# Performance work log

Measured on AMD Instinct MI355X. Metric: run time of the kernel, lower is better.

## Reference

```python
import jax, jax.numpy as jnp
import numpy as np

LEAKY_SLOPE = 0.01  # torch nn.LeakyReLU default


def leaky_relu(x):
    return jnp.where(x >= 0, x, LEAKY_SLOPE * x)


def rgcn_conv(x, edge_index, edge_type, w_rel, w_root, b_conv):
    # PyG RGCNConv: out = x @ W_root + b + sum_r mean_{edges of rel r into i}(x_src @ W_r)
    n = x.shape[0]
    src, dst = edge_index[0], edge_index[1]
    out = x @ w_root + b_conv
    num_rel = w_rel.shape[0]
    for r in range(num_rel):  # small fixed relation count
        mask = (edge_type == r)
        msg = x[src] @ w_rel[r]                      # [E, H]
        msg = jnp.where(mask[:, None], msg, 0.0)
        agg = jax.ops.segment_sum(msg, dst, num_segments=n)          # [N, H]
        cnt = jax.ops.segment_sum(mask.astype(x.dtype), dst, num_segments=n)
        out = out + agg / jnp.maximum(cnt, 1.0)[:, None]             # mean aggr
    return out


def setup_inputs() -> dict:
    key = jax.random.key(0)
    ks = jax.random.split(key, 10)
    N, E, D_IN, H, OUT, R = 50000, 600000, 768, 128, 3, 2
    s_in = 1.0 / np.sqrt(D_IN)
    s_h = 1.0 / np.sqrt(H)
    return {
        "feature": jax.random.normal(ks[0], (N, D_IN), dtype=jnp.float32),
        "edge_index": jax.random.randint(ks[1], (2, E), 0, N, dtype=jnp.int64),
        "edge_type": jax.random.randint(ks[2], (E,), 0, R, dtype=jnp.int64),
        "w_in": jax.random.uniform(ks[3], (D_IN, H), jnp.float32, -s_in, s_in),
        "b_in": jax.random.uniform(ks[4], (H,), jnp.float32, -s_in, s_in),
        "w_rel": jax.random.uniform(ks[5], (R, H, H), jnp.float32, -s_h, s_h),
        "w_root": jax.random.uniform(ks[6], (H, H), jnp.float32, -s_h, s_h),
        "b_conv": jnp.zeros((H,), jnp.float32),
        "w_out": jax.random.uniform(ks[7], (H, OUT), jnp.float32, -s_h, s_h),
        "b_out": jax.random.uniform(ks[8], (OUT,), jnp.float32, -s_h, s_h),
    }


def reference(feature, edge_index, edge_type, w_in, b_in, w_rel, w_root, b_conv, w_out, b_out):
    x = leaky_relu(feature @ w_in + b_in)
    # NOTE: original forward applies rgcn1 twice (shared weights); dropout is
    # identity at inference; rgcn2/linear_relu_output1 are unused.
    x = rgcn_conv(x, edge_index, edge_type, w_rel, w_root, b_conv)
    x = rgcn_conv(x, edge_index, edge_type, w_rel, w_root, b_conv)
    return x @ w_out + b_out
```

## Files before the change

### kernel.cpp

```cpp
#include <hip/hip_runtime.h>

#define H 128
#define CAP 64

typedef _Float16 f16x8 __attribute__((ext_vector_type(8)));
typedef _Float16 f16x2 __attribute__((ext_vector_type(2)));
typedef float    f32x4 __attribute__((ext_vector_type(4)));

__global__ __launch_bounds__(256) void prep_all(const float* __restrict__ w_in,
    const float* __restrict__ w_root, const float* __restrict__ w_rel,
    const float* __restrict__ b_conv, const float* __restrict__ w_out,
    const float* __restrict__ b_out, _Float16* __restrict__ wInT,
    _Float16* __restrict__ wcatT, float* __restrict__ wfin,
    float* __restrict__ bfin, int K, int OUT)
{
    int idx = blockIdx.x * 256 + threadIdx.x;
    int tot1 = K * H;
    if (idx < tot1) {
        int k = idx >> 7, c = idx & 127;
        int o = ((k >> 3) << 10) + (c << 3) + (k & 7);
        wInT[o] = (_Float16)w_in[idx];
        return;
    }
    int i2 = idx - tot1;
    if (i2 < H * 384) {
        int c = i2 / 384, k = i2 - c * 384;
        float v;
        if (k < 128)      v = w_root[(size_t)k * H + c];
        else if (k < 256) v = w_rel[(size_t)(k - 128) * H + c];
        else              v = w_rel[(size_t)H * H + (size_t)(k - 256) * H + c];
        wcatT[i2] = (_Float16)v;
        return;
    }
    int i3 = i2 - H * 384;
    int nw = 3 * H * OUT;
    if (i3 < nw) {
        int mk = i3 / OUT, c = i3 - mk * OUT;
        int m = mk >> 7, k = mk & 127;
        const float* W = (m == 0) ? w_root : (w_rel + (size_t)(m - 1) * H * H);
        float s = 0.f;
        for (int j = 0; j < H; j++)
            s += W[(size_t)k * H + j] * w_out[(size_t)j * OUT + c];
        wfin[(size_t)mk * OUT + c] = s;
    } else if (i3 < nw + OUT) {
        int c = i3 - nw;
        float s = b_out[c];
        for (int j = 0; j < H; j++) s += b_conv[j] * w_out[(size_t)j * OUT + c];
        bfin[c] = s;
    }
}

__device__ __forceinline__ f16x8 cvt8(float4 v0, float4 v1) {
    f16x8 t;
    t[0] = (_Float16)v0.x; t[1] = (_Float16)v0.y; t[2] = (_Float16)v0.z; t[3] = (_Float16)v0.w;
    t[4] = (_Float16)v1.x; t[5] = (_Float16)v1.y; t[6] = (_Float16)v1.z; t[7] = (_Float16)v1.w;
    return t;
}

__global__ __launch_bounds__(256, 2) void gemm_hist(const float* __restrict__ A,
    const _Float16* __restrict__ WP, const float* __restrict__ bias,
    _Float16* __restrict__ C16, int M, int K, int ldc, int gemmBlocks,
    const int* __restrict__ esrc, const int* __restrict__ edst,
    const int* __restrict__ et, int* __restrict__ cnt, int* __restrict__ elist,
    int E, int N)
{
    __shared__ float As[2][4][2048];

    if ((int)blockIdx.x >= gemmBlocks) {
        int e = (blockIdx.x - gemmBlocks) * 256 + threadIdx.x;
        if (e < E) {
            int s = esrc[e], d = edst[e], t = et[e];
            int b = t * N + d;
            int pos = atomicAdd(&cnt[b], 1);
            if (pos < CAP)
                __builtin_nontemporal_store(s, &elist[(size_t)b * CAP + pos]);
        }
        return;
    }

    const int tid = threadIdx.x;
    const int w   = tid >> 6;
    const int l   = tid & 63;
    const int l15 = l & 15;
    const int q   = l >> 4;
    const int brow = blockIdx.x * 64;
    const int wr   = w * 16;

    const int lh  = l >> 5;
    const int l31 = l & 31;

    const _Float16* bp = WP + ((size_t)q * H + l15) * 8;

    float bj[8];
#pragma unroll
    for (int j = 0; j < 8; j++) bj[j] = bias[j * 16 + l15];

    f32x4 acc[8];
    const f32x4 z4 = {0.f, 0.f, 0.f, 0.f};
#pragma unroll
    for (int j = 0; j < 8; j++) acc[j] = z4;

    const int chunks = K / 128;

#define STAGE(c, nbuf)                                                          \
    {                                                                           \
        _Pragma("unroll")                                                       \
        for (int i = 0; i < 8; i++) {                                           \
            int r  = 2 * i + lh;                                                \
            int gr = brow + wr + r; if (gr >= M) gr = M - 1;                    \
            int cg = l31 ^ (r & 7);                                             \
            const float* ga = A + (size_t)gr * K + (c) * 128 + cg * 4;          \
            __builtin_amdgcn_global_load_lds(                                   \
                (const __attribute__((address_space(1))) void*)ga,              \
                (__attribute__((address_space(3))) void*)&As[nbuf][w][i * 256], \
                16, 0, 0);                                                      \
        }                                                                       \
    }

    STAGE(0, 0);
    __syncthreads();

    for (int c = 0; c < chunks; c++) {
        if (c + 1 < chunks) STAGE(c + 1, (c + 1) & 1);

        const float* wbuf = As[c & 1][w];
#pragma unroll
        for (int ks = 0; ks < 4; ks++) {
            const int sl = ks * 4 + q;
            const int xr = l15 & 7;
            const int p0 = (2 * sl) ^ xr;
            const int p1 = (2 * sl + 1) ^ xr;
            float4 lo = *(const float4*)&wbuf[l15 * 128 + p0 * 4];
            float4 hi = *(const float4*)&wbuf[l15 * 128 + p1 * 4];
            f16x8 af = cvt8(lo, hi);
            const _Float16* bks = bp + (size_t)(c * 4 + ks) * 4096;
            f16x8 bf[8];
#pragma unroll
            for (int j = 0; j < 8; j++) bf[j] = *(const f16x8*)(bks + j * 128);
#pragma unroll
            for (int j = 0; j < 8; j++)
                acc[j] = __builtin_amdgcn_mfma_f32_16x16x32_f16(af, bf[j], acc[j], 0, 0, 0);
        }
        __syncthreads();
    }
#undef STAGE

#pragma unroll
    for (int rg = 0; rg < 4; rg++) {
        int row = brow + wr + q * 4 + rg;
        if (row < M) {
#pragma unroll
            for (int j = 0; j < 8; j++) {
                float v = acc[j][rg] + bj[j];
                v = (v >= 0.f) ? v : 0.01f * v;
                C16[(size_t)row * ldc + j * 16 + l15] = (_Float16)v;
            }
        }
    }
}

__global__ __launch_bounds__(256) void fused_l1(const _Float16* __restrict__ X1,
    const _Float16* __restrict__ WT, const float* __restrict__ bias,
    const int* __restrict__ elist, const int* __restrict__ cnt,
    _Float16* __restrict__ X2, int N)
{
    __shared__ _Float16 Ml[16][264];

    const int w   = threadIdx.x >> 6;
    const int l   = threadIdx.x & 63;
    const int l15 = l & 15;
    const int q   = l >> 4;
    const int r0  = blockIdx.x * 16;

    const int eo   = l >> 4;
    const int e2   = eo & 1;
    const int half = l >> 5;
    const int c8   = l15 * 8;

    const f16x8 zv = {};
#pragma unroll
    for (int i = 0; i < 4; i++) {
        const int rl = w * 4 + i;
        const int r  = r0 + rl;
        float acc[8];
#pragma unroll
        for (int j = 0; j < 8; j++) acc[j] = 0.f;
        float inv = 0.f;
        if (r < N) {
            int dr = cnt[(size_t)half * N + r];
            int d  = dr < CAP ? dr : CAP;
            inv = dr > 0 ? 1.f / (float)dr : 0.f;
            const int* lst = elist + ((size_t)half * N + r) * CAP;
            for (int p = e2; p < d; p += 8) {
                int p1 = p + 2, p2 = p + 4, p3 = p + 6;
                int s0 = lst[p];
                f16x8 v0 = *(const f16x8*)&X1[(size_t)s0 * H + c8];
                f16x8 v1 = zv, v2 = zv, v3 = zv;
                if (p1 < d) { int s = lst[p1]; v1 = *(const f16x8*)&X1[(size_t)s * H + c8]; }
                if (p2 < d) { int s = lst[p2]; v2 = *(const f16x8*)&X1[(size_t)s * H + c8]; }
                if (p3 < d) { int s = lst[p3]; v3 = *(const f16x8*)&X1[(size_t)s * H + c8]; }
#pragma unroll
                for (int j = 0; j < 8; j++)
                    acc[j] += (float)v0[j] + (float)v1[j] + (float)v2[j] + (float)v3[j];
            }
        }
#pragma unroll
        for (int j = 0; j < 8; j++) {
            acc[j] += __shfl_xor(acc[j], 16);
            acc[j] *= inv;
        }
        if (r < N && (eo == 0 || eo == 2)) {
            f16x8 o;
#pragma unroll
            for (int j = 0; j < 8; j++) o[j] = (_Float16)acc[j];
            *(f16x8*)&Ml[rl][half * 128 + c8] = o;
        }
    }
    __syncthreads();

    int gr = r0 + l15; if (gr >= N) gr = N - 1;
    f16x8 xf[12];
    {
        const _Float16* xp = X1 + (size_t)gr * H + q * 8;
#pragma unroll
        for (int c = 0; c < 4; c++) xf[c] = *(const f16x8*)(xp + c * 32);
#pragma unroll
        for (int c = 4; c < 12; c++) xf[c] = *(const f16x8*)&Ml[l15][(c - 4) * 32 + q * 8];
    }

    const f32x4 z4 = {0.f, 0.f, 0.f, 0.f};
#pragma unroll
    for (int cf = 0; cf < 2; cf++) {
        const int col = w * 32 + cf * 16 + l15;
        f16x8 bf[12];
        const _Float16* wpp = WT + (size_t)col * 384 + q * 8;
#pragma unroll
        for (int c = 0; c < 12; c++) bf[c] = *(const f16x8*)(wpp + c * 32);
        f32x4 a0 = z4;
#pragma unroll
        for (int c = 0; c < 12; c++)
            a0 = __builtin_amdgcn_mfma_f32_16x16x32_f16(xf[c], bf[c], a0, 0, 0, 0);
        const float bj = bias[col];
#pragma unroll
        for (int rg = 0; rg < 4; rg++) {
            int row = r0 + q * 4 + rg;
            if (row < N) X2[(size_t)row * H + col] = (_Float16)(a0[rg] + bj);
        }
    }
}

__global__ __launch_bounds__(256) void proj9(const _Float16* __restrict__ X2,
    const float* __restrict__ wfin, float* __restrict__ P, int N)
{
    int row = blockIdx.x * 4 + (threadIdx.x >> 6);
    int l   = threadIdx.x & 63;
    if (row >= N) return;

    f16x2 xv = *(const f16x2*)&X2[(size_t)row * H + 2 * l];
    float x0 = (float)xv[0], x1 = (float)xv[1];

    float p[9];
#pragma unroll
    for (int c = 0; c < 9; c++) {
        int m  = (c < 3) ? 1 : (c < 6) ? 2 : 0;
        int cc = (c < 3) ? c : (c < 6) ? c - 3 : c - 6;
        float w0 = wfin[(size_t)(m * H + 2 * l) * 3 + cc];
        float w1 = wfin[(size_t)(m * H + 2 * l + 1) * 3 + cc];
        p[c] = x0 * w0 + x1 * w1;
    }
#pragma unroll
    for (int off = 1; off <= 32; off <<= 1)
#pragma unroll
        for (int c = 0; c < 9; c++) p[c] += __shfl_xor(p[c], off);

    if (l == 0) {
        float* pr = P + (size_t)row * 12;
#pragma unroll
        for (int c = 0; c < 3; c++) {
            pr[c]     = p[c];
            pr[4 + c] = p[3 + c];
            pr[8 + c] = p[6 + c];
        }
    }
}

__global__ __launch_bounds__(256) void gather_fin(const float* __restrict__ P,
    const int* __restrict__ elist, const int* __restrict__ cnt,
    const float* __restrict__ bfin, float* __restrict__ out, int N)
{
    int i = blockIdx.x * 256 + threadIdx.x;
    if (i >= N) return;

    float o0 = P[(size_t)i * 12 + 8] + bfin[0];
    float o1 = P[(size_t)i * 12 + 9] + bfin[1];
    float o2 = P[(size_t)i * 12 + 10] + bfin[2];

#pragma unroll
    for (int r = 0; r < 2; r++) {
        int dr = cnt[(size_t)r * N + i];
        int d  = dr < CAP ? dr : CAP;
        float inv = dr > 0 ? 1.f / (float)dr : 0.f;
        const int* lst = elist + ((size_t)r * N + i) * CAP;
        float s0 = 0.f, s1 = 0.f, s2 = 0.f;
        int p = 0;
        for (; p + 3 < d; p += 4) {
            int a = lst[p], b = lst[p + 1], c = lst[p + 2], e = lst[p + 3];
            float4 va = *(const float4*)&P[(size_t)a * 12 + r * 4];
            float4 vb = *(const float4*)&P[(size_t)b * 12 + r * 4];
            float4 vc = *(const float4*)&P[(size_t)c * 12 + r * 4];
            float4 ve = *(const float4*)&P[(size_t)e * 12 + r * 4];
            s0 += va.x + vb.x + vc.x + ve.x;
            s1 += va.y + vb.y + vc.y + ve.y;
            s2 += va.z + vb.z + vc.z + ve.z;
        }
        for (; p < d; p++) {
            int a = lst[p];
            float4 va = *(const float4*)&P[(size_t)a * 12 + r * 4];
            s0 += va.x; s1 += va.y; s2 += va.z;
        }
        o0 += s0 * inv; o1 += s1 * inv; o2 += s2 * inv;
    }
    out[(size_t)i * 3 + 0] = o0;
    out[(size_t)i * 3 + 1] = o1;
    out[(size_t)i * 3 + 2] = o2;
}

template<int MODE>
__global__ __launch_bounds__(256) void gather_k(const _Float16* __restrict__ X,
    int ldx, _Float16* __restrict__ Mout, const int* __restrict__ elist,
    const int* __restrict__ cnt, int N,
    const float* __restrict__ wfin, const float* __restrict__ bfin,
    float* __restrict__ out)
{
    int wv = blockIdx.x * 4 + (threadIdx.x >> 6);
    int l  = threadIdx.x & 63;
    if (wv >= N) return;

    const int eo   = l >> 4;
    const int e2   = eo & 1;
    const int half = l >> 5;
    const int c8   = (l & 15) * 8;

    int dr = cnt[(size_t)half * N + wv];
    int d  = dr < CAP ? dr : CAP;
    float inv = dr > 0 ? 1.f / (float)dr : 0.f;
    const int* lst = elist + ((size_t)half * N + wv) * CAP;

    float acc[8];
#pragma unroll
    for (int j = 0; j < 8; j++) acc[j] = 0.f;

    const f16x8 zv = {};
    for (int p = e2; p < d; p += 8) {
        int p1 = p + 2, p2 = p + 4, p3 = p + 6;
        int s0 = lst[p];
        f16x8 v0 = *(const f16x8*)&X[(size_t)s0 * ldx + c8];
        f16x8 v1 = zv, v2 = zv, v3 = zv;
        if (p1 < d) { int s = lst[p1]; v1 = *(const f16x8*)&X[(size_t)s * ldx + c8]; }
        if (p2 < d) { int s = lst[p2]; v2 = *(const f16x8*)&X[(size_t)s * ldx + c8]; }
        if (p3 < d) { int s = lst[p3]; v3 = *(const f16x8*)&X[(size_t)s * ldx + c8]; }
#pragma unroll
        for (int j = 0; j < 8; j++)
            acc[j] += (float)v0[j] + (float)v1[j] + (float)v2[j] + (float)v3[j];
    }

#pragma unroll
    for (int j = 0; j < 8; j++) {
        acc[j] += __shfl_xor(acc[j], 16);
        acc[j] *= inv;
    }

    if (MODE == 0) {
        if (eo == 0 || eo == 2) {
            f16x8 o;
#pragma unroll
            for (int j = 0; j < 8; j++) o[j] = (_Float16)acc[j];
            *(f16x8*)&Mout[(size_t)wv * 256 + half * 128 + c8] = o;
        }
    }
}

__global__ __launch_bounds__(512) void gemm_cat(const _Float16* __restrict__ X1,
    const _Float16* __restrict__ Mt, const _Float16* __restrict__ WT,
    const float* __restrict__ bias, _Float16* __restrict__ X2, int M, int mtiles)
{
    const int w   = threadIdx.x >> 6;
    const int l   = threadIdx.x & 63;
    const int l15 = l & 15;
    const int q   = l >> 4;
    const int col = w * 16 + l15;

    f16x8 bf[12];
    {
        const _Float16* wpp = WT + (size_t)col * 384 + q * 8;
#pragma unroll
        for (int c = 0; c < 12; c++) bf[c] = *(const f16x8*)(wpp + c * 32);
    }
    const float bj = bias[col];

    int t = blockIdx.x;
    if (t >= mtiles) return;
    f16x8 xf[12];
    {
        const _Float16* xp = X1 + ((size_t)t * 16 + l15) * 128 + q * 8;
        const _Float16* mp = Mt + ((size_t)t * 16 + l15) * 256 + q * 8;
#pragma unroll
        for (int c = 0; c < 4; c++) xf[c] = *(const f16x8*)(xp + c * 32);
#pragma unroll
        for (int c = 4; c < 12; c++) xf[c] = *(const f16x8*)(mp + (c - 4) * 32);
    }

    const f32x4 z4 = {0.f, 0.f, 0.f, 0.f};
    while (true) {
        int tn = t + gridDim.x;
        bool more = tn < mtiles;
        f16x8 xnf[12];
        if (more) {
            const _Float16* xp = X1 + ((size_t)tn * 16 + l15) * 128 + q * 8;
            const _Float16* mp = Mt + ((size_t)tn * 16 + l15) * 256 + q * 8;
#pragma unroll
            for (int c = 0; c < 4; c++) xnf[c] = *(const f16x8*)(xp + c * 32);
#pragma unroll
            for (int c = 4; c < 12; c++) xnf[c] = *(const f16x8*)(mp + (c - 4) * 32);
        }

        f32x4 a0 = z4;
#pragma unroll
        for (int c = 0; c < 12; c++)
            a0 = __builtin_amdgcn_mfma_f32_16x16x32_f16(xf[c], bf[c], a0, 0, 0, 0);

#pragma unroll
        for (int rg = 0; rg < 4; rg++) {
            int row = t * 16 + q * 4 + rg;
            if (row < M) X2[(size_t)row * 128 + col] = (_Float16)(a0[rg] + bj);
        }
        if (!more) break;
        t = tn;
#pragma unroll
        for (int c = 0; c < 12; c++) xf[c] = xnf[c];
    }
}

__global__ __launch_bounds__(256) void proj_generic(const _Float16* __restrict__ X2,
    const _Float16* __restrict__ Mt, const float* __restrict__ wfin,
    const float* __restrict__ bfin, float* __restrict__ out, int N, int OUT)
{
    int row = blockIdx.x * 4 + (threadIdx.x >> 6);
    int l = threadIdx.x & 63;
    if (row >= N) return;
    float xv[6];
#pragma unroll
    for (int i = 0; i < 6; i++) {
        int k = l * 6 + i;
        xv[i] = (k < 128) ? (float)X2[(size_t)row * 128 + k]
                          : (float)Mt[(size_t)row * 256 + (k - 128)];
    }
    for (int c = 0; c < OUT; c++) {
        float p = 0.f;
#pragma unroll
        for (int i = 0; i < 6; i++) p += xv[i] * wfin[(size_t)(l * 6 + i) * OUT + c];
        for (int off = 32; off > 0; off >>= 1) p += __shfl_down(p, off);
        if (l == 0) out[(size_t)row * OUT + c] = p + bfin[c];
    }
}

extern "C" void kernel_launch(void* const* d_in, const int* in_sizes, int n_in,
                              void* d_out, int out_size, void* d_ws, size_t ws_size,
                              hipStream_t stream) {
    const float* feature = (const float*)d_in[0];
    const int*   ei      = (const int*)d_in[1];
    const int*   et      = (const int*)d_in[2];
    const float* w_in    = (const float*)d_in[3];
    const float* b_in    = (const float*)d_in[4];
    const float* w_rel   = (const float*)d_in[5];
    const float* w_root  = (const float*)d_in[6];
    const float* b_conv  = (const float*)d_in[7];
    const float* w_out   = (const float*)d_in[8];
    const float* b_out   = (const float*)d_in[9];

    const int HH   = in_sizes[4];
    const int D_IN = in_sizes[3] / HH;
    const int N    = in_sizes[0] / D_IN;
    const int E    = in_sizes[1] / 2;
    const int OUT  = in_sizes[9];

    char* base = (char*)d_ws;
    _Float16* wInT  = (_Float16*)base;
    _Float16* wcatT = wInT + (size_t)D_IN * HH;
    _Float16* X1    = wcatT + (size_t)HH * 384;
    _Float16* X2    = X1 + (size_t)N * HH;
    _Float16* Mt    = X2 + (size_t)N * HH;
    float* Pt       = (float*)(Mt + (size_t)N * 256);
    float* wfin     = Pt + (size_t)N * 12;
    float* bfin     = wfin + (size_t)3 * HH * (OUT > 0 ? OUT : 1);
    int* cnt        = (int*)(bfin + ((OUT + 3) & ~3));
    int* elist      = cnt + (size_t)2 * N;

    hipMemsetAsync(cnt, 0, sizeof(int) * (size_t)2 * N, stream);
    {
        int ptot = D_IN * HH + HH * 384 + 3 * HH * OUT + OUT;
        prep_all<<<(ptot + 255) / 256, 256, 0, stream>>>(
            w_in, w_root, w_rel, b_conv, w_out, b_out,
            wInT, wcatT, wfin, bfin, D_IN, OUT);
    }

    const int gemmBlocks = (N + 63) / 64;
    const int histBlocks = (E + 255) / 256;
    gemm_hist<<<gemmBlocks + histBlocks, 256, 0, stream>>>(
        feature, wInT, b_in, X1, N, D_IN, HH, gemmBlocks,
        ei, ei + E, et, cnt, elist, E, N);

    const int mtiles  = (N + 15) / 16;
    const int gblocks = (N + 3) / 4;

    if (OUT == 3) {
        fused_l1<<<mtiles, 256, 0, stream>>>(X1, wcatT, b_conv, elist, cnt, X2, N);
        proj9<<<gblocks, 256, 0, stream>>>(X2, wfin, Pt, N);
        gather_fin<<<(N + 255) / 256, 256, 0, stream>>>(Pt, elist, cnt, bfin,
                                                        (float*)d_out, N);
    } else {
        gather_k<0><<<gblocks, 256, 0, stream>>>(X1, 128, Mt, elist, cnt, N,
                                                 nullptr, nullptr, nullptr);
        gemm_cat<<<1024, 512, 0, stream>>>(X1, Mt, wcatT, b_conv, X2, N, mtiles);
        gather_k<0><<<gblocks, 256, 0, stream>>>(X2, 128, Mt, elist, cnt, N,
                                                 nullptr, nullptr, nullptr);
        proj_generic<<<gblocks, 256, 0, stream>>>(X2, Mt, wfin, bfin,
                                                  (float*)d_out, N, OUT);
    }
}
```

Measured before the change: 401.2 us.

## Fuse 9-column output projection into layer-1 GEMM epilogue, drop X2 round trip

The layer-1 fused gather+GEMM kernel now projects its 128-wide result directly onto the nine final projection columns in registers. It reduces them across lanes with shuffles and shared-memory atomics and writes only the 12-float P rows. This removes the proj9 launch and the fp16 X2 write and reread. In exchange the epilogue gains register pressure from a 4x9 accumulator array, shuffle reductions and LDS atomics. X2 is also no longer rounded to fp16 before the projection, which changes numerics slightly.

```diff
diff --git a/kernel.cpp b/kernel.cpp
--- a/kernel.cpp
+++ b/kernel.cpp
@@ -161,13 +161,15 @@
 
 __global__ __launch_bounds__(256) void fused_l1(const _Float16* __restrict__ X1,
     const _Float16* __restrict__ WT, const float* __restrict__ bias,
-    const int* __restrict__ elist, const int* __restrict__ cnt,
-    _Float16* __restrict__ X2, int N)
+    const float* __restrict__ wfin, const int* __restrict__ elist,
+    const int* __restrict__ cnt, float* __restrict__ P, int N)
 {
     __shared__ _Float16 Ml[16][264];
-
-    const int w   = threadIdx.x >> 6;
-    const int l   = threadIdx.x & 63;
+    __shared__ float Pl[16][9];
+
+    const int tid = threadIdx.x;
+    const int w   = tid >> 6;
+    const int l   = tid & 63;
     const int l15 = l & 15;
     const int q   = l >> 4;
     const int r0  = blockIdx.x * 16;
@@ -176,6 +178,8 @@
     const int e2   = eo & 1;
     const int half = l >> 5;
     const int c8   = l15 * 8;
+
+    if (tid < 144) Pl[tid / 9][tid % 9] = 0.f;
 
     const f16x8 zv = {};
 #pragma unroll
@@ -228,6 +232,12 @@
         for (int c = 4; c < 12; c++) xf[c] = *(const f16x8*)&Ml[l15][(c - 4) * 32 + q * 8];
     }
 
+    float pp[4][9];
+#pragma unroll
+    for (int rg = 0; rg < 4; rg++)
+#pragma unroll
+        for (int c = 0; c < 9; c++) pp[rg][c] = 0.f;
+
     const f32x4 z4 = {0.f, 0.f, 0.f, 0.f};
 #pragma unroll
     for (int cf = 0; cf < 2; cf++) {
@@ -241,45 +251,45 @@
         for (int c = 0; c < 12; c++)
             a0 = __builtin_amdgcn_mfma_f32_16x16x32_f16(xf[c], bf[c], a0, 0, 0, 0);
         const float bj = bias[col];
+        const float* w0 = wfin + (size_t)(0 * H + col) * 3;
+        const float* w1 = wfin + (size_t)(1 * H + col) * 3;
+        const float* w2 = wfin + (size_t)(2 * H + col) * 3;
 #pragma unroll
         for (int rg = 0; rg < 4; rg++) {
-            int row = r0 + q * 4 + rg;
-            if (row < N) X2[(size_t)row * H + col] = (_Float16)(a0[rg] + bj);
-        }
-    }
-}
-
-__global__ __launch_bounds__(256) void proj9(const _Float16* __restrict__ X2,
-    const float* __restrict__ wfin, float* __restrict__ P, int N)
-{
-    int row = blockIdx.x * 4 + (threadIdx.x >> 6);
-    int l   = threadIdx.x & 63;
-    if (row >= N) return;
-
-    f16x2 xv = *(const f16x2*)&X2[(size_t)row * H + 2 * l];
-    float x0 = (float)xv[0], x1 = (float)xv[1];
-
-    float p[9];
-#pragma unroll
-    for (int c = 0; c < 9; c++) {
-        int m  = (c < 3) ? 1 : (c < 6) ? 2 : 0;
-        int cc = (c < 3) ? c : (c < 6) ? c - 3 : c - 6;
-        float w0 = wfin[(size_t)(m * H + 2 * l) * 3 + cc];
-        float w1 = wfin[(size_t)(m * H + 2 * l + 1) * 3 + cc];
-        p[c] = x0 * w0 + x1 * w1;
-    }
-#pragma unroll
-    for (int off = 1; off <= 32; off <<= 1)
-#pragma unroll
-        for (int c = 0; c < 9; c++) p[c] += __shfl_xor(p[c], off);
-
-    if (l == 0) {
-        float* pr = P + (size_t)row * 12;
-#pragma unroll
-        for (int c = 0; c < 3; c++) {
-            pr[c]     = p[c];
-            pr[4 + c] = p[3 + c];
-            pr[8 + c] = p[6 + c];
+            float v = a0[rg] + bj;
+#pragma unroll
+            for (int c3 = 0; c3 < 3; c3++) {
+                pp[rg][c3]     += v * w1[c3];
+                pp[rg][3 + c3] += v * w2[c3];
+                pp[rg][6 + c3] += v * w0[c3];
+            }
+        }
+    }
+
+#pragma unroll
+    for (int rg = 0; rg < 4; rg++)
+#pragma unroll
+        for (int c = 0; c < 9; c++) {
+            pp[rg][c] += __shfl_xor(pp[rg][c], 1);
+            pp[rg][c] += __shfl_xor(pp[rg][c], 2);
+            pp[rg][c] += __shfl_xor(pp[rg][c], 4);
+            pp[rg][c] += __shfl_xor(pp[rg][c], 8);
+        }
+    if (l15 < 9) {
+        const int c = l15;
+#pragma unroll
+        for (int rg = 0; rg < 4; rg++)
+            atomicAdd(&Pl[q * 4 + rg][c], pp[rg][c]);
+    }
+    __syncthreads();
+
+    if (tid < 144) {
+        int rl = tid / 9, c = tid % 9;
+        int row = r0 + rl;
+        if (row < N) {
+            int slice = (c < 3) ? 0 : (c < 6) ? 4 : 8;
+            int cc    = (c < 3) ? c : (c < 6) ? c - 3 : c - 6;
+            P[(size_t)row * 12 + slice + cc] = Pl[rl][c];
         }
     }
 }
@@ -514,8 +524,8 @@
     const int gblocks = (N + 3) / 4;
 
     if (OUT == 3) {
-        fused_l1<<<mtiles, 256, 0, stream>>>(X1, wcatT, b_conv, elist, cnt, X2, N);
-        proj9<<<gblocks, 256, 0, stream>>>(X2, wfin, Pt, N);
+        fused_l1<<<mtiles, 256, 0, stream>>>(X1, wcatT, b_conv, wfin,
+                                             elist, cnt, Pt, N);
         gather_fin<<<(N + 255) / 256, 256, 0, stream>>>(Pt, elist, cnt, bfin,
                                                         (float*)d_out, N);
     } else {
```

Measured after the change: 408.6 us. No clear change (+1.8%).
